# Performance work log

Measured on AMD Instinct MI355X. Metric: run time of the kernel, lower is better.

Reference implementation:

```python
import jax, jax.numpy as jnp
import numpy as np

N_NODES = 20000
N_EDGES = 320000
N_GRAPHS = 512
IN_FEATS = 128
HID = 256
RDKIT_IN = 2048
RDK_H1, RDK_H2 = 1024, 512
COMB_H1, COMB_H2 = 1024, 512
N_TASKS = 1
EPS = 1e-5


def _lin(k, fan_in, fan_out):
    return jax.random.normal(k, (fan_in, fan_out), jnp.float32) / np.float32(np.sqrt(fan_in))


def setup_inputs() -> dict:
    key = jax.random.key(0)
    ks = jax.random.split(key, 24)
    inp = {}
    inp["node_feats"] = jax.random.normal(ks[0], (N_NODES, IN_FEATS), jnp.float32)
    inp["rdkit_feats"] = jax.random.normal(ks[1], (N_GRAPHS, RDKIT_IN), jnp.float32)
    inp["src"] = jax.random.randint(ks[2], (N_EDGES,), 0, N_NODES, dtype=jnp.int32)
    inp["dst"] = jax.random.randint(ks[3], (N_EDGES,), 0, N_NODES, dtype=jnp.int32)
    # sorted graph ids; first N_GRAPHS entries guarantee every graph has >=1 node
    gid = jnp.concatenate([jnp.arange(N_GRAPHS, dtype=jnp.int32),
                           jax.random.randint(ks[4], (N_NODES - N_GRAPHS,), 0, N_GRAPHS, dtype=jnp.int32)])
    inp["node_gid"] = jnp.sort(gid)
    # GCN layer params (GraphConv W,b + residual Linear + BatchNorm gamma/beta)
    dims = [(IN_FEATS, HID), (HID, HID)]
    for i, (fi, fo) in enumerate(dims, start=1):
        inp[f"W{i}"] = _lin(ks[4 + 4 * i], fi, fo)
        inp[f"b{i}"] = jnp.zeros((fo,), jnp.float32)
        inp[f"rW{i}"] = _lin(ks[5 + 4 * i], fi, fo)
        inp[f"rb{i}"] = jnp.zeros((fo,), jnp.float32)
        inp[f"g{i}"] = jnp.ones((fo,), jnp.float32)
        inp[f"be{i}"] = jnp.zeros((fo,), jnp.float32)
    inp["aw_W"] = _lin(ks[16], HID, 1)
    inp["aw_b"] = jnp.zeros((1,), jnp.float32)
    inp["rk_W1"] = _lin(ks[17], RDKIT_IN, RDK_H1)
    inp["rk_b1"] = jnp.zeros((RDK_H1,), jnp.float32)
    inp["rk_W2"] = _lin(ks[18], RDK_H1, RDK_H2)
    inp["rk_b2"] = jnp.zeros((RDK_H2,), jnp.float32)
    comb_in = RDK_H2 + 2 * HID
    inp["c_W1"] = _lin(ks[19], comb_in, COMB_H1)
    inp["c_b1"] = jnp.zeros((COMB_H1,), jnp.float32)
    inp["c_W2"] = _lin(ks[20], COMB_H1, COMB_H2)
    inp["c_b2"] = jnp.zeros((COMB_H2,), jnp.float32)
    inp["c_W3"] = _lin(ks[21], COMB_H2, N_TASKS)
    inp["c_b3"] = jnp.zeros((N_TASKS,), jnp.float32)
    return inp


def _gcn_layer(h, src, dst, W, b, rW, rb, g, be):
    # GraphConv, norm='none': sum incoming messages of (X W), then bias + relu
    m = h @ W                                                    # [N, out]
    agg = jax.ops.segment_sum(m[src], dst, num_segments=h.shape[0])
    new = jax.nn.relu(agg + b)
    # residual Linear with activation (dgllife GCNLayer)
    new = new + jax.nn.relu(h @ rW + rb)
    # BatchNorm1d over nodes (training-mode batch stats; dropout in eval = identity)
    mu = new.mean(axis=0)
    var = new.var(axis=0)
    return g * (new - mu) * jax.lax.rsqrt(var + EPS) + be


def reference(node_feats, rdkit_feats, src, dst, node_gid,
              W1, b1, rW1, rb1, g1, be1,
              W2, b2, rW2, rb2, g2, be2,
              aw_W, aw_b, rk_W1, rk_b1, rk_W2, rk_b2,
              c_W1, c_b1, c_W2, c_b2, c_W3, c_b3):
    h = _gcn_layer(node_feats, src, dst, W1, b1, rW1, rb1, g1, be1)
    h = _gcn_layer(h, src, dst, W2, b2, rW2, rb2, g2, be2)
    # WeightedSumAndMax readout
    w = jax.nn.sigmoid(h @ aw_W + aw_b)                          # [N, 1]
    hg_sum = jax.ops.segment_sum(h * w, node_gid, num_segments=N_GRAPHS)
    hg_max = jax.ops.segment_max(h, node_gid, num_segments=N_GRAPHS)
    graph_feats = jnp.concatenate([hg_sum, hg_max], axis=1)       # [B, 2*HID]
    # RDKit encoder MLP
    r = jax.nn.relu(rdkit_feats @ rk_W1 + rk_b1)
    r = jax.nn.relu(r @ rk_W2 + rk_b2)
    z = jnp.concatenate([graph_feats, r], axis=1)
    z = jax.nn.relu(z @ c_W1 + c_b1)
    z = jax.nn.relu(z @ c_W2 + c_b2)
    return z @ c_W3 + c_b3                                       # [B, n_tasks]
```

## Files before the change

### kernel.cpp

```cpp
#include <hip/hip_runtime.h>
#include <hip/hip_bf16.h>
#include <cstdint>
#include <cstddef>

#define N_NODES 20000
#define N_EDGES 320000
#define N_GRAPHS 512
#define IN_FEATS 128
#define HID 256

typedef __bf16 bhalf;
typedef __bf16 bhalf8 __attribute__((ext_vector_type(8)));
typedef __bf16 bhalf4 __attribute__((ext_vector_type(4)));
typedef __bf16 bhalf2 __attribute__((ext_vector_type(2)));
typedef float f32x4 __attribute__((ext_vector_type(4)));

__device__ __forceinline__ int2 xcd_swz(int bx, int by, int nbx, int nby)
{
    int lid = by * nbx + bx;
    int nwg = nbx * nby;
    int q = nwg >> 3, r = nwg & 7;
    int xcd = lid & 7, loc = lid >> 3;
    int s = (xcd < r ? xcd * (q + 1) : r * (q + 1) + (xcd - r) * q) + loc;
    return make_int2(s % nbx, s / nbx);
}

template<int RELU, int OUTBF16>
__global__ __launch_bounds__(256) void gemm_mfma(const bhalf* __restrict__ A,
                                                 const bhalf* __restrict__ Bt,
                                                 void* __restrict__ Cv,
                                                 const float* __restrict__ bias,
                                                 int M, int K, int ldc)
{
    __shared__ bhalf As[64 * 64];
    __shared__ bhalf Bs[64 * 64];

    const int t = threadIdx.x;
    const int lane = t & 63, wid = t >> 6;
    const int wm0 = (wid >> 1) * 32, wn0 = (wid & 1) * 32;
    int2 bsw = xcd_swz(blockIdx.x, blockIdx.y, gridDim.x, gridDim.y);
    const int m0 = bsw.y * 64, n0 = bsw.x * 64;
    const int S = gridDim.z, kz = blockIdx.z;
    const int Ks = K / S;

    const int srow = t >> 2;
    const int sc0 = (t & 3) << 3;

    f32x4 acc[2][2] = {};
    uint4 ra0, ra1, rb0, rb1;

    const bool mok = (m0 + srow) < M;
    const bhalf* Abase = A + (size_t)(m0 + srow) * K + (size_t)kz * Ks;
    const bhalf* Bbase = Bt + (size_t)(n0 + srow) * K + (size_t)kz * Ks;

    ra0 = mok ? *(const uint4*)(Abase + sc0)      : make_uint4(0u,0u,0u,0u);
    ra1 = mok ? *(const uint4*)(Abase + sc0 + 32) : make_uint4(0u,0u,0u,0u);
    rb0 = *(const uint4*)(Bbase + sc0);
    rb1 = *(const uint4*)(Bbase + sc0 + 32);

    const int swz = (srow & 7) << 3;
    for (int k0 = 0; k0 < Ks; k0 += 64) {
        __syncthreads();
        *(uint4*)&As[srow * 64 + (sc0 ^ swz)]        = ra0;
        *(uint4*)&As[srow * 64 + ((sc0 + 32) ^ swz)] = ra1;
        *(uint4*)&Bs[srow * 64 + (sc0 ^ swz)]        = rb0;
        *(uint4*)&Bs[srow * 64 + ((sc0 + 32) ^ swz)] = rb1;
        __syncthreads();
        if (k0 + 64 < Ks) {
            const bhalf* An = Abase + k0 + 64;
            const bhalf* Bn = Bbase + k0 + 64;
            ra0 = mok ? *(const uint4*)(An + sc0)      : make_uint4(0u,0u,0u,0u);
            ra1 = mok ? *(const uint4*)(An + sc0 + 32) : make_uint4(0u,0u,0u,0u);
            rb0 = *(const uint4*)(Bn + sc0);
            rb1 = *(const uint4*)(Bn + sc0 + 32);
        }
#pragma unroll
        for (int kb = 0; kb < 2; ++kb) {
            const int kc = kb * 32 + (lane >> 4) * 8;
            bhalf8 af[2], bfr[2];
#pragma unroll
            for (int i = 0; i < 2; ++i) {
                int rA = wm0 + i * 16 + (lane & 15);
                af[i] = *(const bhalf8*)&As[rA * 64 + (kc ^ ((rA & 7) << 3))];
                int rB = wn0 + i * 16 + (lane & 15);
                bfr[i] = *(const bhalf8*)&Bs[rB * 64 + (kc ^ ((rB & 7) << 3))];
            }
#pragma unroll
            for (int mi = 0; mi < 2; ++mi)
#pragma unroll
                for (int ni = 0; ni < 2; ++ni)
                    acc[mi][ni] = __builtin_amdgcn_mfma_f32_16x16x32_bf16(
                        af[mi], bfr[ni], acc[mi][ni], 0, 0, 0);
        }
    }

#pragma unroll
    for (int mi = 0; mi < 2; ++mi)
#pragma unroll
        for (int ni = 0; ni < 2; ++ni) {
            int col = n0 + wn0 + ni * 16 + (lane & 15);
            f32x4 v = acc[mi][ni];
            if (S > 1) {
#pragma unroll
                for (int r = 0; r < 4; ++r) {
                    int row = m0 + wm0 + mi * 16 + (lane >> 4) * 4 + r;
                    if (row < M)
                        ((float*)Cv)[((size_t)kz * M + row) * ldc + col] = v[r];
                }
            } else {
                float bb = bias ? bias[col] : 0.f;
#pragma unroll
                for (int r = 0; r < 4; ++r) {
                    int row = m0 + wm0 + mi * 16 + (lane >> 4) * 4 + r;
                    if (row < M) {
                        float x = v[r] + bb;
                        if (RELU) x = fmaxf(x, 0.f);
                        if (OUTBF16) ((bhalf*)Cv)[(size_t)row * ldc + col] = (bhalf)x;
                        else         ((float*)Cv)[(size_t)row * ldc + col] = x;
                    }
                }
            }
        }
}

template<int BN>
__global__ __launch_bounds__(256) void gcn_gemm_fused(const bhalf* __restrict__ Aagg,
                                                      const bhalf* __restrict__ Ax,
                                                      const bhalf* __restrict__ BW,
                                                      const bhalf* __restrict__ BrW,
                                                      const float* __restrict__ b,
                                                      const float* __restrict__ rb,
                                                      bhalf* __restrict__ vout,
                                                      float* __restrict__ stats,
                                                      int M, int K,
                                                      const float* __restrict__ bnstats,
                                                      const float* __restrict__ bng,
                                                      const float* __restrict__ bnbe,
                                                      float inv_n)
{
    __shared__ bhalf As[64 * 64];
    __shared__ bhalf Bs[64 * 64];
    __shared__ float ssum[64], ssq[64];
    __shared__ float bnS[256], bnB[256];

    const int t = threadIdx.x;
    const int lane = t & 63, wid = t >> 6;
    const int wm0 = (wid >> 1) * 32, wn0 = (wid & 1) * 32;
    int2 bsw = xcd_swz(blockIdx.x, blockIdx.y, gridDim.x, gridDim.y);
    const int m0 = bsw.y * 64, n0 = bsw.x * 64;

    const int srow = t >> 2;
    const int sc0 = (t & 3) << 3;
    const int nk = K >> 6;

    if (BN && t < K) {
        float mu = bnstats[t] * inv_n;
        float rs = rsqrtf(bnstats[K + t] * inv_n - mu * mu + 1e-5f);
        float s = bng[t] * rs;
        bnS[t] = s;
        bnB[t] = bnbe[t] - mu * s;
    }

    f32x4 accM[2][2] = {};
    f32x4 accR[2][2] = {};
    uint4 ra0, ra1, rb0, rb1;

    const bool mok = (m0 + srow) < M;
    const bhalf* A0r = Aagg + (size_t)(m0 + srow) * K;
    const bhalf* A1r = Ax + (size_t)(m0 + srow) * K;
    const bhalf* B0r = BW + (size_t)(n0 + srow) * K;
    const bhalf* B1r = BrW + (size_t)(n0 + srow) * K;

    ra0 = mok ? *(const uint4*)(A0r + sc0)      : make_uint4(0u,0u,0u,0u);
    ra1 = mok ? *(const uint4*)(A0r + sc0 + 32) : make_uint4(0u,0u,0u,0u);
    rb0 = *(const uint4*)(B0r + sc0);
    rb1 = *(const uint4*)(B0r + sc0 + 32);

    const int swz = (srow & 7) << 3;
    const int total = 2 * nk;
    if (BN) __syncthreads();
    for (int ii = 0; ii < total; ++ii) {
        __syncthreads();
        if (BN && ii >= nk) {
            int kb0 = ((ii - nk) << 6) + sc0;
            bhalf8 a0 = *(bhalf8*)&ra0, a1 = *(bhalf8*)&ra1;
#pragma unroll
            for (int j = 0; j < 8; ++j) {
                a0[j] = (bhalf)((float)a0[j] * bnS[kb0 + j] + bnB[kb0 + j]);
                a1[j] = (bhalf)((float)a1[j] * bnS[kb0 + 32 + j] + bnB[kb0 + 32 + j]);
            }
            ra0 = *(uint4*)&a0; ra1 = *(uint4*)&a1;
        }
        *(uint4*)&As[srow * 64 + (sc0 ^ swz)]        = ra0;
        *(uint4*)&As[srow * 64 + ((sc0 + 32) ^ swz)] = ra1;
        *(uint4*)&Bs[srow * 64 + (sc0 ^ swz)]        = rb0;
        *(uint4*)&Bs[srow * 64 + ((sc0 + 32) ^ swz)] = rb1;
        __syncthreads();
        int jj = ii + 1;
        if (jj < total) {
            bool seln = jj >= nk;
            int kk = (seln ? jj - nk : jj) << 6;
            const bhalf* Ab = (seln ? A1r : A0r) + kk;
            const bhalf* Bb = (seln ? B1r : B0r) + kk;
            ra0 = mok ? *(const uint4*)(Ab + sc0)      : make_uint4(0u,0u,0u,0u);
            ra1 = mok ? *(const uint4*)(Ab + sc0 + 32) : make_uint4(0u,0u,0u,0u);
            rb0 = *(const uint4*)(Bb + sc0);
            rb1 = *(const uint4*)(Bb + sc0 + 32);
        }
        const bool selc = ii >= nk;
#pragma unroll
        for (int kb = 0; kb < 2; ++kb) {
            const int kc = kb * 32 + (lane >> 4) * 8;
            bhalf8 af[2], bfr[2];
#pragma unroll
            for (int i = 0; i < 2; ++i) {
                int rA = wm0 + i * 16 + (lane & 15);
                af[i] = *(const bhalf8*)&As[rA * 64 + (kc ^ ((rA & 7) << 3))];
                int rB = wn0 + i * 16 + (lane & 15);
                bfr[i] = *(const bhalf8*)&Bs[rB * 64 + (kc ^ ((rB & 7) << 3))];
            }
            if (!selc) {
#pragma unroll
                for (int mi = 0; mi < 2; ++mi)
#pragma unroll
                    for (int ni = 0; ni < 2; ++ni)
                        accM[mi][ni] = __builtin_amdgcn_mfma_f32_16x16x32_bf16(
                            af[mi], bfr[ni], accM[mi][ni], 0, 0, 0);
            } else {
#pragma unroll
                for (int mi = 0; mi < 2; ++mi)
#pragma unroll
                    for (int ni = 0; ni < 2; ++ni)
                        accR[mi][ni] = __builtin_amdgcn_mfma_f32_16x16x32_bf16(
                            af[mi], bfr[ni], accR[mi][ni], 0, 0, 0);
            }
        }
    }

    if (t < 64) { ssum[t] = 0.f; ssq[t] = 0.f; }
    __syncthreads();
    float sloc[2] = {0.f, 0.f}, s2loc[2] = {0.f, 0.f};
#pragma unroll
    for (int ni = 0; ni < 2; ++ni) {
        int cl = wn0 + ni * 16 + (lane & 15);
        int c = n0 + cl;
        float bb = b[c], rbb = rb[c];
#pragma unroll
        for (int mi = 0; mi < 2; ++mi) {
            f32x4 a0v = accM[mi][ni], a1v = accR[mi][ni];
#pragma unroll
            for (int r = 0; r < 4; ++r) {
                int row = m0 + wm0 + mi * 16 + (lane >> 4) * 4 + r;
                if (row < M) {
                    float x = fmaxf(a0v[r] + bb, 0.f) + fmaxf(a1v[r] + rbb, 0.f);
                    vout[(size_t)row * HID + c] = (bhalf)x;
                    sloc[ni] += x;
                    s2loc[ni] += x * x;
                }
            }
        }
        atomicAdd(&ssum[cl], sloc[ni]);
        atomicAdd(&ssq[cl], s2loc[ni]);
    }
    __syncthreads();
    if (t < 64) {
        atomicAdd(&stats[n0 + t], ssum[t]);
        atomicAdd(&stats[HID + n0 + t], ssq[t]);
    }
}

template<int RELU, int OUTBF16>
__global__ __launch_bounds__(256) void splitk_combine(const float* __restrict__ part,
                                                      int S, int M, int N, int ldo,
                                                      const float* __restrict__ bias,
                                                      void* __restrict__ outv)
{
    int i = blockIdx.x * blockDim.x + threadIdx.x;
    int n4 = N >> 2;
    if (i >= M * n4) return;
    int row = i / n4, c4 = (i - row * n4) << 2;
    float4 s = make_float4(0.f, 0.f, 0.f, 0.f);
    for (int z = 0; z < S; ++z) {
        float4 p = *(const float4*)(part + ((size_t)z * M + row) * N + c4);
        s.x += p.x; s.y += p.y; s.z += p.z; s.w += p.w;
    }
    float4 bb = *(const float4*)(bias + c4);
    s.x += bb.x; s.y += bb.y; s.z += bb.z; s.w += bb.w;
    if (RELU) {
        s.x = fmaxf(s.x, 0.f); s.y = fmaxf(s.y, 0.f);
        s.z = fmaxf(s.z, 0.f); s.w = fmaxf(s.w, 0.f);
    }
    if (OUTBF16) {
        bhalf4 o = {(bhalf)s.x, (bhalf)s.y, (bhalf)s.z, (bhalf)s.w};
        *(bhalf4*)((bhalf*)outv + (size_t)row * ldo + c4) = o;
    } else {
        *(float4*)((float*)outv + (size_t)row * ldo + c4) = s;
    }
}

__global__ __launch_bounds__(128) void splitk_combine_dot(const float* __restrict__ part,
                                                          int S, int M, int N,
                                                          const float* __restrict__ bias,
                                                          const float* __restrict__ W3,
                                                          const float* __restrict__ b3,
                                                          float* __restrict__ out)
{
    int row = blockIdx.x, t = threadIdx.x;
    int c4 = t << 2;
    float4 s = make_float4(0.f, 0.f, 0.f, 0.f);
    for (int z = 0; z < S; ++z) {
        float4 p = *(const float4*)(part + ((size_t)z * M + row) * N + c4);
        s.x += p.x; s.y += p.y; s.z += p.z; s.w += p.w;
    }
    float4 bb = *(const float4*)(bias + c4);
    float4 w = *(const float4*)(W3 + c4);
    float d = fmaxf(s.x + bb.x, 0.f) * w.x + fmaxf(s.y + bb.y, 0.f) * w.y
            + fmaxf(s.z + bb.z, 0.f) * w.z + fmaxf(s.w + bb.w, 0.f) * w.w;
#pragma unroll
    for (int off = 32; off > 0; off >>= 1) d += __shfl_xor(d, off);
    __shared__ float ws2[2];
    if ((t & 63) == 0) ws2[t >> 6] = d;
    __syncthreads();
    if (t == 0) out[row] = ws2[0] + ws2[1] + b3[0];
}

struct WEnt { const float* src; bhalf* dst; int K; int N; int tiles_end; };
struct PrepTab {
    WEnt e[8];
    const float* ca; bhalf* coa; int n4a;
    const float* cb; bhalf* cob; int n4b;
    uint4* zbase; int zn;
};

#define WTILES 4288
#define CONVB  3524

__global__ __launch_bounds__(256) void prep_batch(PrepTab tab)
{
    __shared__ float tile[32][33];
    int tb = blockIdx.x;
    int t = threadIdx.x;
    if (tb < WTILES) {
        int idx = 0;
#pragma unroll
        for (int i = 0; i < 8; ++i)
            if (tb >= tab.e[i].tiles_end) idx = i + 1;
        const WEnt& E = tab.e[idx];
        int t0 = idx ? tab.e[idx - 1].tiles_end : 0;
        int lt = tb - t0;
        int tX = E.N >> 5;
        int bx = (lt % tX) << 5;
        int by = (lt / tX) << 5;
        int tx = t & 31, ty = t >> 5;
#pragma unroll
        for (int i = 0; i < 32; i += 8)
            tile[ty + i][tx] = E.src[(size_t)(by + ty + i) * E.N + bx + tx];
        __syncthreads();
#pragma unroll
        for (int i = 0; i < 32; i += 8)
            E.dst[(size_t)(bx + ty + i) * E.K + by + tx] = (bhalf)tile[tx][ty + i];
    } else if (tb < WTILES + CONVB) {
        int i = (tb - WTILES) * 256 + t;
        const float* s; bhalf* d; int j;
        if (i < tab.n4a) { s = tab.ca; d = tab.coa; j = i; }
        else { j = i - tab.n4a; if (j >= tab.n4b) return; s = tab.cb; d = tab.cob; }
        float4 v = ((const float4*)s)[j];
        bhalf4 o = {(bhalf)v.x, (bhalf)v.y, (bhalf)v.z, (bhalf)v.w};
        ((bhalf4*)d)[j] = o;
    } else {
        int j = (tb - WTILES - CONVB) * 256 + t;
        if (j < tab.zn) tab.zbase[j] = make_uint4(0u, 0u, 0u, 0u);
    }
}

__global__ void csr_count(const int* __restrict__ dst, int* __restrict__ counts)
{
    int e = blockIdx.x * blockDim.x + threadIdx.x;
    if (e >= N_EDGES) return;
    atomicAdd(&counts[dst[e]], 1);
}

__global__ __launch_bounds__(256) void csr_scan_a(const int* __restrict__ counts,
                                                  int* __restrict__ bsum)
{
    int i = blockIdx.x * 256 + threadIdx.x;
    int v = (i < N_NODES) ? counts[i] : 0;
#pragma unroll
    for (int off = 32; off > 0; off >>= 1) v += __shfl_down(v, off);
    __shared__ int ws[4];
    if ((threadIdx.x & 63) == 0) ws[threadIdx.x >> 6] = v;
    __syncthreads();
    if (threadIdx.x == 0) bsum[blockIdx.x] = ws[0] + ws[1] + ws[2] + ws[3];
}

__global__ __launch_bounds__(256) void csr_scan_c(const int* __restrict__ counts,
                                                  const int* __restrict__ bsum, int nb,
                                                  int* __restrict__ offsets)
{
    int t = threadIdx.x, b = blockIdx.x;
    int i = b * 256 + t;
    int v = (i < N_NODES) ? counts[i] : 0;
    int x = v;
#pragma unroll
    for (int off = 1; off < 64; off <<= 1) {
        int y = __shfl_up(x, off);
        if ((t & 63) >= off) x += y;
    }
    __shared__ int wsum[4];
    __shared__ int tmp[128];
    __shared__ int addsh;
    if ((t & 63) == 63) wsum[t >> 6] = x;
    if (t < 128) tmp[t] = (t < nb) ? bsum[t] : 0;
    __syncthreads();
    if (t == 0) {
        int a = 0;
        for (int j = 0; j < b; ++j) a += tmp[j];
        addsh = a;
    }
    __syncthreads();
    int add = addsh;
    for (int w = 0; w < (t >> 6); ++w) add += wsum[w];
    int excl = x - v + add;
    if (i < N_NODES) offsets[i] = excl;
    if (i == N_NODES - 1) offsets[N_NODES] = excl + v;
}

__global__ void csr_fill(const int* __restrict__ src, const int* __restrict__ dst,
                         const int* __restrict__ offsets, int* __restrict__ cursor,
                         int* __restrict__ eidx)
{
    int e = blockIdx.x * blockDim.x + threadIdx.x;
    if (e >= N_EDGES) return;
    int d = dst[e];
    int slot = offsets[d] + atomicAdd(&cursor[d], 1);
    eidx[slot] = src[e];
}

__global__ void csr_sort_wave(const int* __restrict__ offsets, int* __restrict__ eidx)
{
    int gidx = blockIdx.x * blockDim.x + threadIdx.x;
    int n = gidx >> 6, lane = gidx & 63;
    if (n >= N_NODES) return;
    int lo = offsets[n], hi = offsets[n + 1];
    int cnt = hi - lo;
    if (cnt <= 1) return;
    if (cnt <= 64) {
        int v = (lane < cnt) ? eidx[lo + lane] : 0x7fffffff;
        int rank = 0;
        for (int j = 0; j < cnt; ++j) {
            int vj = __shfl(v, j);
            if (vj < v || (vj == v && j < lane)) ++rank;
        }
        if (lane < cnt) eidx[lo + rank] = v;
    } else if (lane == 0) {
        for (int i = lo + 1; i < hi; ++i) {
            int v = eidx[i]; int j = i - 1;
            while (j >= lo && eidx[j] > v) { eidx[j + 1] = eidx[j]; --j; }
            eidx[j + 1] = v;
        }
    }
}

__global__ __launch_bounds__(256) void edge_gather1(const bhalf* __restrict__ m,
                                                    const int* __restrict__ offsets,
                                                    const int* __restrict__ eidx,
                                                    bhalf* __restrict__ agg)
{
    int gidx = blockIdx.x * blockDim.x + threadIdx.x;
    int n = gidx >> 6, lane = gidx & 63;
    if (n >= N_NODES) return;
    int lo = offsets[n], hi = offsets[n + 1];
    int sub = lane >> 4;
    int colb = (lane & 15) * 8;
    float acc[8] = {};
    int i = lo;
    for (; i + 8 <= hi; i += 8) {
        bhalf8 v0 = *(const bhalf8*)(m + (size_t)eidx[i + sub] * IN_FEATS + colb);
        bhalf8 v1 = *(const bhalf8*)(m + (size_t)eidx[i + 4 + sub] * IN_FEATS + colb);
#pragma unroll
        for (int j = 0; j < 8; ++j) acc[j] += (float)v0[j] + (float)v1[j];
    }
    if (i + 4 <= hi) {
        bhalf8 v0 = *(const bhalf8*)(m + (size_t)eidx[i + sub] * IN_FEATS + colb);
#pragma unroll
        for (int j = 0; j < 8; ++j) acc[j] += (float)v0[j];
        i += 4;
    }
    if (i < hi && sub < hi - i) {
        bhalf8 v0 = *(const bhalf8*)(m + (size_t)eidx[i + sub] * IN_FEATS + colb);
#pragma unroll
        for (int j = 0; j < 8; ++j) acc[j] += (float)v0[j];
    }
#pragma unroll
    for (int j = 0; j < 8; ++j) {
        acc[j] += __shfl_xor(acc[j], 16);
        acc[j] += __shfl_xor(acc[j], 32);
    }
    if (sub == 0) {
        bhalf8 o;
#pragma unroll
        for (int j = 0; j < 8; ++j) o[j] = (bhalf)acc[j];
        *(bhalf8*)(agg + (size_t)n * IN_FEATS + colb) = o;
    }
}

__global__ __launch_bounds__(256) void edge_gather2_bn(const bhalf* __restrict__ m,
                                                       const int* __restrict__ offsets,
                                                       const int* __restrict__ eidx,
                                                       const float* __restrict__ bnstats,
                                                       const float* __restrict__ bng,
                                                       const float* __restrict__ bnbe,
                                                       float inv_n,
                                                       bhalf* __restrict__ agg)
{
    int gidx = blockIdx.x * blockDim.x + threadIdx.x;
    int n = gidx >> 6, lane = gidx & 63;
    if (n >= N_NODES) return;
    int lo = offsets[n], hi = offsets[n + 1];
    int sub = lane >> 5;
    int colb = (lane & 31) * 8;
    float acc[8] = {};
    int i = lo;
    for (; i + 8 <= hi; i += 8) {
        bhalf8 v0 = *(const bhalf8*)(m + (size_t)eidx[i + sub] * HID + colb);
        bhalf8 v1 = *(const bhalf8*)(m + (size_t)eidx[i + 2 + sub] * HID + colb);
        bhalf8 v2 = *(const bhalf8*)(m + (size_t)eidx[i + 4 + sub] * HID + colb);
        bhalf8 v3 = *(const bhalf8*)(m + (size_t)eidx[i + 6 + sub] * HID + colb);
#pragma unroll
        for (int j = 0; j < 8; ++j)
            acc[j] += ((float)v0[j] + (float)v1[j]) + ((float)v2[j] + (float)v3[j]);
    }
    for (; i + 2 <= hi; i += 2) {
        bhalf8 v0 = *(const bhalf8*)(m + (size_t)eidx[i + sub] * HID + colb);
#pragma unroll
        for (int j = 0; j < 8; ++j) acc[j] += (float)v0[j];
    }
    if (i < hi && sub == 0) {
        bhalf8 v0 = *(const bhalf8*)(m + (size_t)eidx[i] * HID + colb);
#pragma unroll
        for (int j = 0; j < 8; ++j) acc[j] += (float)v0[j];
    }
#pragma unroll
    for (int j = 0; j < 8; ++j)
        acc[j] += __shfl_xor(acc[j], 32);
    if (sub == 0) {
        float d = (float)(hi - lo);
        bhalf8 o;
#pragma unroll
        for (int j = 0; j < 8; ++j) {
            int c = colb + j;
            float mu = bnstats[c] * inv_n;
            float rs = rsqrtf(bnstats[HID + c] * inv_n - mu * mu + 1e-5f);
            float s = bng[c] * rs;
            float tt = bnbe[c] - mu * s;
            o[j] = (bhalf)(acc[j] * s + d * tt);
        }
        *(bhalf8*)(agg + (size_t)n * HID + colb) = o;
    }
}

__global__ __launch_bounds__(256) void bn_row_aw(const bhalf* __restrict__ v,
                                                 const float* __restrict__ stats,
                                                 float inv_n,
                                                 const float* __restrict__ g,
                                                 const float* __restrict__ be,
                                                 bhalf* __restrict__ outb,
                                                 const float* __restrict__ awW,
                                                 const float* __restrict__ awb,
                                                 float* __restrict__ w)
{
    int gidx = blockIdx.x * blockDim.x + threadIdx.x;
    int n = gidx >> 6, lane = gidx & 63;
    if (n >= N_NODES) return;
    int col = lane * 4;
    bhalf4 vv = *(const bhalf4*)(v + (size_t)n * HID + col);
    float4 sm = *(const float4*)(stats + col);
    float4 sq = *(const float4*)(stats + HID + col);
    float4 gg = *(const float4*)(g + col);
    float4 bb = *(const float4*)(be + col);
    float mux = sm.x * inv_n, muy = sm.y * inv_n, muz = sm.z * inv_n, muw = sm.w * inv_n;
    float rsx = rsqrtf(sq.x * inv_n - mux * mux + 1e-5f);
    float rsy = rsqrtf(sq.y * inv_n - muy * muy + 1e-5f);
    float rsz = rsqrtf(sq.z * inv_n - muz * muz + 1e-5f);
    float rsw = rsqrtf(sq.w * inv_n - muw * muw + 1e-5f);
    float4 o;
    o.x = gg.x * ((float)vv.x - mux) * rsx + bb.x;
    o.y = gg.y * ((float)vv.y - muy) * rsy + bb.y;
    o.z = gg.z * ((float)vv.z - muz) * rsz + bb.z;
    o.w = gg.w * ((float)vv.w - muw) * rsw + bb.w;
    bhalf4 ob = {(bhalf)o.x, (bhalf)o.y, (bhalf)o.z, (bhalf)o.w};
    *(bhalf4*)(outb + (size_t)n * HID + col) = ob;
    float4 wv = *(const float4*)(awW + col);
    float d = o.x * wv.x + o.y * wv.y + o.z * wv.z + o.w * wv.w;
#pragma unroll
    for (int off = 32; off > 0; off >>= 1) d += __shfl_xor(d, off);
    if (lane == 0) w[n] = 1.f / (1.f + expf(-(d + awb[0])));
}

__global__ __launch_bounds__(256) void readout(const bhalf* __restrict__ h,
                                               const float* __restrict__ w,
                                               const int* __restrict__ gid,
                                               bhalf* __restrict__ z)
{
    int g = blockIdx.x, col = threadIdx.x;
    int lo = 0, hi = N_NODES;
    while (lo < hi) { int mid = (lo + hi) >> 1; if (gid[mid] < g) lo = mid + 1; else hi = mid; }
    int start = lo;
    hi = N_NODES;
    while (lo < hi) { int mid = (lo + hi) >> 1; if (gid[mid] <= g) lo = mid + 1; else hi = mid; }
    int end = lo;
    float s = 0.f, mx = -INFINITY;
    for (int n = start; n < end; ++n) {
        float v = (float)h[(size_t)n * HID + col];
        s = fmaf(v, w[n], s);
        mx = fmaxf(mx, v);
    }
    z[(size_t)g * 1024 + col] = (bhalf)s;
    z[(size_t)g * 1024 + HID + col] = (bhalf)mx;
}

extern "C" void kernel_launch(void* const* d_in, const int* in_sizes, int n_in,
                              void* d_out, int out_size, void* d_ws, size_t ws_size,
                              hipStream_t stream)
{
    (void)in_sizes; (void)n_in; (void)out_size; (void)ws_size;

    const float* node_feats = (const float*)d_in[0];
    const float* rdkit      = (const float*)d_in[1];
    const int*   src        = (const int*)d_in[2];
    const int*   dst        = (const int*)d_in[3];
    const int*   gid        = (const int*)d_in[4];
    const float* W1  = (const float*)d_in[5];
    const float* b1  = (const float*)d_in[6];
    const float* rW1 = (const float*)d_in[7];
    const float* rb1 = (const float*)d_in[8];
    const float* g1  = (const float*)d_in[9];
    const float* be1 = (const float*)d_in[10];
    const float* W2  = (const float*)d_in[11];
    const float* b2  = (const float*)d_in[12];
    const float* rW2 = (const float*)d_in[13];
    const float* rb2 = (const float*)d_in[14];
    const float* g2  = (const float*)d_in[15];
    const float* be2 = (const float*)d_in[16];
    const float* aw_W  = (const float*)d_in[17];
    const float* aw_b  = (const float*)d_in[18];
    const float* rk_W1 = (const float*)d_in[19];
    const float* rk_b1 = (const float*)d_in[20];
    const float* rk_W2 = (const float*)d_in[21];
    const float* rk_b2 = (const float*)d_in[22];
    const float* c_W1  = (const float*)d_in[23];
    const float* c_b1  = (const float*)d_in[24];
    const float* c_W2  = (const float*)d_in[25];
    const float* c_b2  = (const float*)d_in[26];
    const float* c_W3  = (const float*)d_in[27];
    const float* c_b3  = (const float*)d_in[28];

    float* out = (float*)d_out;

    const size_t NODE = (size_t)N_NODES * HID;
    bhalf* nfb   = (bhalf*)d_ws;
    bhalf* h2b   = nfb + (size_t)N_NODES * IN_FEATS;
    bhalf* aggb  = h2b + NODE;
    bhalf* vb    = aggb + NODE;
    bhalf* vb2   = vb + NODE;
    bhalf* W1cat = vb2 + NODE;
    bhalf* W2cat = W1cat + 512 * 128;
    bhalf* rkW1t = W2cat + 512 * 256;
    bhalf* rkW2t = rkW1t + 2048 * 1024;
    bhalf* cW1t  = rkW2t + 1024 * 512;
    bhalf* cW2t  = cW1t + 1024 * 1024;
    bhalf* rdkb  = cW2t + 1024 * 512;
    float* stats1 = (float*)(rdkb + 512 * 2048);
    float* stats2 = stats1 + 512;
    int*   counts = (int*)(stats2 + 512);
    int*   cursor = counts + N_NODES;
    float* wbuf   = (float*)(cursor + N_NODES);
    int*   offsets = (int*)(wbuf + N_NODES);
    int*   eidx    = offsets + N_NODES + 1;
    int*   bsum    = eidx + N_EDGES;
    bhalf* rkhb  = (bhalf*)(bsum + 128);
    bhalf* zb    = rkhb + 512 * 1024;
    bhalf* ch1b  = zb + 512 * 1024;
    float* spart = (float*)(ch1b + 512 * 1024);

    dim3 blk(256);
    const int EPB = (N_EDGES + 255) / 256;
    const int NPB = (N_NODES + 255) / 256;
    const int NWAVE = (N_NODES * 64) / 256;
    dim3 gfused(HID / 64, (N_NODES + 63) / 64);

    PrepTab tab;
    tab.e[0] = {W1,    W1cat,             128, 256,   32};
    tab.e[1] = {rW1,   W1cat + 256 * 128, 128, 256,   64};
    tab.e[2] = {W2,    W2cat,             256, 256,  128};
    tab.e[3] = {rW2,   W2cat + 256 * 256, 256, 256,  192};
    tab.e[4] = {rk_W1, rkW1t,            2048, 1024, 2240};
    tab.e[5] = {rk_W2, rkW2t,            1024, 512,  2752};
    tab.e[6] = {c_W1,  cW1t,             1024, 1024, 3776};
    tab.e[7] = {c_W2,  cW2t,             1024, 512,  4288};
    tab.ca = node_feats; tab.coa = nfb;  tab.n4a = N_NODES * IN_FEATS / 4;
    tab.cb = rdkit;      tab.cob = rdkb; tab.n4b = 512 * 2048 / 4;
    tab.zbase = (uint4*)stats1;
    tab.zn = (1024 + 2 * N_NODES) / 4;
    const int ZB = (tab.zn + 255) / 256;
    prep_batch<<<WTILES + CONVB + ZB, blk, 0, stream>>>(tab);

    csr_count<<<EPB, blk, 0, stream>>>(dst, counts);
    csr_scan_a<<<NPB, blk, 0, stream>>>(counts, bsum);
    csr_scan_c<<<NPB, blk, 0, stream>>>(counts, bsum, NPB, offsets);
    csr_fill<<<EPB, blk, 0, stream>>>(src, dst, offsets, cursor, eidx);
    csr_sort_wave<<<NWAVE, blk, 0, stream>>>(offsets, eidx);

    edge_gather1<<<NWAVE, blk, 0, stream>>>(nfb, offsets, eidx, aggb);
    gcn_gemm_fused<0><<<gfused, blk, 0, stream>>>(aggb, nfb, W1cat, W1cat + 256 * 128,
                                                  b1, rb1, vb, stats1, N_NODES, IN_FEATS,
                                                  nullptr, nullptr, nullptr, 0.f);

    edge_gather2_bn<<<NWAVE, blk, 0, stream>>>(vb, offsets, eidx,
                                               stats1, g1, be1, 1.0f / N_NODES, aggb);
    gcn_gemm_fused<1><<<gfused, blk, 0, stream>>>(aggb, vb, W2cat, W2cat + 256 * 256,
                                                  b2, rb2, vb2, stats2, N_NODES, HID,
                                                  stats1, g1, be1, 1.0f / N_NODES);
    bn_row_aw<<<NWAVE, blk, 0, stream>>>(vb2, stats2, 1.0f / N_NODES, g2, be2,
                                         h2b, aw_W, aw_b, wbuf);

    readout<<<N_GRAPHS, HID, 0, stream>>>(h2b, wbuf, gid, zb);

    gemm_mfma<0,0><<<dim3(16, 8, 4), blk, 0, stream>>>(rdkb, rkW1t, spart, nullptr,
                                                       512, 2048, 1024);
    splitk_combine<1,1><<<512, blk, 0, stream>>>(spart, 4, 512, 1024, 1024, rk_b1, rkhb);
    gemm_mfma<0,0><<<dim3(8, 8, 8), blk, 0, stream>>>(rkhb, rkW2t, spart, nullptr,
                                                      512, 1024, 512);
    splitk_combine<1,1><<<256, blk, 0, stream>>>(spart, 8, 512, 512, 1024, rk_b2, zb + 512);

    gemm_mfma<0,0><<<dim3(16, 8, 4), blk, 0, stream>>>(zb, cW1t, spart, nullptr,
                                                       512, 1024, 1024);
    splitk_combine<1,1><<<512, blk, 0, stream>>>(spart, 4, 512, 1024, 1024, c_b1, ch1b);
    gemm_mfma<0,0><<<dim3(8, 8, 8), blk, 0, stream>>>(ch1b, cW2t, spart, nullptr,
                                                      512, 1024, 512);
    splitk_combine_dot<<<512, 128, 0, stream>>>(spart, 8, 512, 512, c_b2, c_W3, c_b3, out);
}
```

Baseline: 230.2 us.

## Fuse BN2 and attention weights into readout, fold split-K combine into next GEMM

```diff
diff --git a/kernel.cpp b/kernel.cpp
--- a/kernel.cpp
+++ b/kernel.cpp
@@ -25,11 +25,12 @@
     return make_int2(s % nbx, s / nbx);
 }
 
-template<int RELU, int OUTBF16>
-__global__ __launch_bounds__(256) void gemm_mfma(const bhalf* __restrict__ A,
+template<int RELU, int OUTBF16, int CIN>
+__global__ __launch_bounds__(256) void gemm_mfma(const void* __restrict__ Av,
                                                  const bhalf* __restrict__ Bt,
                                                  void* __restrict__ Cv,
                                                  const float* __restrict__ bias,
+                                                 const float* __restrict__ biasA,
                                                  int M, int K, int ldc)
 {
     __shared__ bhalf As[64 * 64];
@@ -49,28 +50,67 @@
     f32x4 acc[2][2] = {};
     uint4 ra0, ra1, rb0, rb1;
 
-    const bool mok = (m0 + srow) < M;
-    const bhalf* Abase = A + (size_t)(m0 + srow) * K + (size_t)kz * Ks;
+    const int grow = m0 + srow;
+    const bool mok = grow < M;
+    const bhalf* Abase = (const bhalf*)Av + (size_t)grow * K + (size_t)kz * Ks;
+    const float* Afb   = (const float*)Av + (size_t)grow * K + (size_t)kz * Ks;
+    const size_t zstr = (size_t)M * K;
     const bhalf* Bbase = Bt + (size_t)(n0 + srow) * K + (size_t)kz * Ks;
 
-    ra0 = mok ? *(const uint4*)(Abase + sc0)      : make_uint4(0u,0u,0u,0u);
-    ra1 = mok ? *(const uint4*)(Abase + sc0 + 32) : make_uint4(0u,0u,0u,0u);
+    if (CIN == 0) {
+        ra0 = mok ? *(const uint4*)(Abase + sc0)      : make_uint4(0u,0u,0u,0u);
+        ra1 = mok ? *(const uint4*)(Abase + sc0 + 32) : make_uint4(0u,0u,0u,0u);
+    }
     rb0 = *(const uint4*)(Bbase + sc0);
     rb1 = *(const uint4*)(Bbase + sc0 + 32);
 
     const int swz = (srow & 7) << 3;
     for (int k0 = 0; k0 < Ks; k0 += 64) {
         __syncthreads();
-        *(uint4*)&As[srow * 64 + (sc0 ^ swz)]        = ra0;
-        *(uint4*)&As[srow * 64 + ((sc0 + 32) ^ swz)] = ra1;
+        if (CIN == 0) {
+            *(uint4*)&As[srow * 64 + (sc0 ^ swz)]        = ra0;
+            *(uint4*)&As[srow * 64 + ((sc0 + 32) ^ swz)] = ra1;
+        } else {
+            int kg = kz * Ks + k0;
+            float a0[8], a1[8];
+#pragma unroll
+            for (int j = 0; j < 8; ++j) {
+                a0[j] = biasA[kg + sc0 + j];
+                a1[j] = biasA[kg + sc0 + 32 + j];
+            }
+            if (mok) {
+#pragma unroll
+                for (int z = 0; z < CIN; ++z) {
+                    const float* p = Afb + (size_t)z * zstr + k0;
+                    float4 q0 = *(const float4*)(p + sc0);
+                    float4 q1 = *(const float4*)(p + sc0 + 4);
+                    float4 q2 = *(const float4*)(p + sc0 + 32);
+                    float4 q3 = *(const float4*)(p + sc0 + 36);
+                    a0[0] += q0.x; a0[1] += q0.y; a0[2] += q0.z; a0[3] += q0.w;
+                    a0[4] += q1.x; a0[5] += q1.y; a0[6] += q1.z; a0[7] += q1.w;
+                    a1[0] += q2.x; a1[1] += q2.y; a1[2] += q2.z; a1[3] += q2.w;
+                    a1[4] += q3.x; a1[5] += q3.y; a1[6] += q3.z; a1[7] += q3.w;
+                }
+            }
+            bhalf8 o0, o1;
+#pragma unroll
+            for (int j = 0; j < 8; ++j) {
+                o0[j] = (bhalf)(mok ? fmaxf(a0[j], 0.f) : 0.f);
+                o1[j] = (bhalf)(mok ? fmaxf(a1[j], 0.f) : 0.f);
+            }
+            *(bhalf8*)&As[srow * 64 + (sc0 ^ swz)]        = o0;
+            *(bhalf8*)&As[srow * 64 + ((sc0 + 32) ^ swz)] = o1;
+        }
         *(uint4*)&Bs[srow * 64 + (sc0 ^ swz)]        = rb0;
         *(uint4*)&Bs[srow * 64 + ((sc0 + 32) ^ swz)] = rb1;
         __syncthreads();
         if (k0 + 64 < Ks) {
-            const bhalf* An = Abase + k0 + 64;
+            if (CIN == 0) {
+                const bhalf* An = Abase + k0 + 64;
+                ra0 = mok ? *(const uint4*)(An + sc0)      : make_uint4(0u,0u,0u,0u);
+                ra1 = mok ? *(const uint4*)(An + sc0 + 32) : make_uint4(0u,0u,0u,0u);
+            }
             const bhalf* Bn = Bbase + k0 + 64;
-            ra0 = mok ? *(const uint4*)(An + sc0)      : make_uint4(0u,0u,0u,0u);
-            ra1 = mok ? *(const uint4*)(An + sc0 + 32) : make_uint4(0u,0u,0u,0u);
             rb0 = *(const uint4*)(Bn + sc0);
             rb1 = *(const uint4*)(Bn + sc0 + 32);
         }
@@ -559,64 +599,47 @@
     }
 }
 
-__global__ __launch_bounds__(256) void bn_row_aw(const bhalf* __restrict__ v,
-                                                 const float* __restrict__ stats,
-                                                 float inv_n,
-                                                 const float* __restrict__ g,
-                                                 const float* __restrict__ be,
-                                                 bhalf* __restrict__ outb,
-                                                 const float* __restrict__ awW,
-                                                 const float* __restrict__ awb,
-                                                 float* __restrict__ w)
-{
-    int gidx = blockIdx.x * blockDim.x + threadIdx.x;
-    int n = gidx >> 6, lane = gidx & 63;
-    if (n >= N_NODES) return;
-    int col = lane * 4;
-    bhalf4 vv = *(const bhalf4*)(v + (size_t)n * HID + col);
-    float4 sm = *(const float4*)(stats + col);
-    float4 sq = *(const float4*)(stats + HID + col);
-    float4 gg = *(const float4*)(g + col);
-    float4 bb = *(const float4*)(be + col);
-    float mux = sm.x * inv_n, muy = sm.y * inv_n, muz = sm.z * inv_n, muw = sm.w * inv_n;
-    float rsx = rsqrtf(sq.x * inv_n - mux * mux + 1e-5f);
-    float rsy = rsqrtf(sq.y * inv_n - muy * muy + 1e-5f);
-    float rsz = rsqrtf(sq.z * inv_n - muz * muz + 1e-5f);
-    float rsw = rsqrtf(sq.w * inv_n - muw * muw + 1e-5f);
-    float4 o;
-    o.x = gg.x * ((float)vv.x - mux) * rsx + bb.x;
-    o.y = gg.y * ((float)vv.y - muy) * rsy + bb.y;
-    o.z = gg.z * ((float)vv.z - muz) * rsz + bb.z;
-    o.w = gg.w * ((float)vv.w - muw) * rsw + bb.w;
-    bhalf4 ob = {(bhalf)o.x, (bhalf)o.y, (bhalf)o.z, (bhalf)o.w};
-    *(bhalf4*)(outb + (size_t)n * HID + col) = ob;
-    float4 wv = *(const float4*)(awW + col);
-    float d = o.x * wv.x + o.y * wv.y + o.z * wv.z + o.w * wv.w;
-#pragma unroll
-    for (int off = 32; off > 0; off >>= 1) d += __shfl_xor(d, off);
-    if (lane == 0) w[n] = 1.f / (1.f + expf(-(d + awb[0])));
-}
-
-__global__ __launch_bounds__(256) void readout(const bhalf* __restrict__ h,
-                                               const float* __restrict__ w,
-                                               const int* __restrict__ gid,
-                                               bhalf* __restrict__ z)
-{
-    int g = blockIdx.x, col = threadIdx.x;
+__global__ __launch_bounds__(256) void readout_bn(const bhalf* __restrict__ v,
+                                                  const float* __restrict__ stats,
+                                                  float inv_n,
+                                                  const float* __restrict__ g,
+                                                  const float* __restrict__ be,
+                                                  const float* __restrict__ awW,
+                                                  const float* __restrict__ awb,
+                                                  const int* __restrict__ gid,
+                                                  bhalf* __restrict__ z)
+{
+    int gr = blockIdx.x, col = threadIdx.x;
+    int lane = col & 63, wid = col >> 6;
+    float mu = stats[col] * inv_n;
+    float rs = rsqrtf(stats[HID + col] * inv_n - mu * mu + 1e-5f);
+    float s = g[col] * rs;
+    float tt = be[col] - mu * s;
+    float aw = awW[col];
+    float ab = awb[0];
     int lo = 0, hi = N_NODES;
-    while (lo < hi) { int mid = (lo + hi) >> 1; if (gid[mid] < g) lo = mid + 1; else hi = mid; }
+    while (lo < hi) { int mid = (lo + hi) >> 1; if (gid[mid] < gr) lo = mid + 1; else hi = mid; }
     int start = lo;
     hi = N_NODES;
-    while (lo < hi) { int mid = (lo + hi) >> 1; if (gid[mid] <= g) lo = mid + 1; else hi = mid; }
+    while (lo < hi) { int mid = (lo + hi) >> 1; if (gid[mid] <= gr) lo = mid + 1; else hi = mid; }
     int end = lo;
-    float s = 0.f, mx = -INFINITY;
+
+    __shared__ float red[4];
+    float sum = 0.f, mx = -INFINITY;
     for (int n = start; n < end; ++n) {
-        float v = (float)h[(size_t)n * HID + col];
-        s = fmaf(v, w[n], s);
-        mx = fmaxf(mx, v);
-    }
-    z[(size_t)g * 1024 + col] = (bhalf)s;
-    z[(size_t)g * 1024 + HID + col] = (bhalf)mx;
+        float h = (float)v[(size_t)n * HID + col] * s + tt;
+        float d = h * aw;
+#pragma unroll
+        for (int off = 32; off > 0; off >>= 1) d += __shfl_xor(d, off);
+        if (lane == 0) red[wid] = d;
+        __syncthreads();
+        float w = 1.f / (1.f + expf(-(red[0] + red[1] + red[2] + red[3] + ab)));
+        __syncthreads();
+        sum = fmaf(h, w, sum);
+        mx = fmaxf(mx, h);
+    }
+    z[(size_t)gr * 1024 + col] = (bhalf)sum;
+    z[(size_t)gr * 1024 + HID + col] = (bhalf)mx;
 }
 
 extern "C" void kernel_launch(void* const* d_in, const int* in_sizes, int n_in,
@@ -659,8 +682,7 @@
 
     const size_t NODE = (size_t)N_NODES * HID;
     bhalf* nfb   = (bhalf*)d_ws;
-    bhalf* h2b   = nfb + (size_t)N_NODES * IN_FEATS;
-    bhalf* aggb  = h2b + NODE;
+    bhalf* aggb  = nfb + (size_t)N_NODES * IN_FEATS;
     bhalf* vb    = aggb + NODE;
     bhalf* vb2   = vb + NODE;
     bhalf* W1cat = vb2 + NODE;
@@ -674,14 +696,12 @@
     float* stats2 = stats1 + 512;
     int*   counts = (int*)(stats2 + 512);
     int*   cursor = counts + N_NODES;
-    float* wbuf   = (float*)(cursor + N_NODES);
-    int*   offsets = (int*)(wbuf + N_NODES);
+    int*   offsets = cursor + N_NODES;
     int*   eidx    = offsets + N_NODES + 1;
     int*   bsum    = eidx + N_EDGES;
-    bhalf* rkhb  = (bhalf*)(bsum + 128);
-    bhalf* zb    = rkhb + 512 * 1024;
-    bhalf* ch1b  = zb + 512 * 1024;
-    float* spart = (float*)(ch1b + 512 * 1024);
+    bhalf* zb    = (bhalf*)(bsum + 128);
+    float* spart = (float*)(zb + 512 * 1024);
+    float* spart2 = spart + 4 * 512 * 1024;
 
     dim3 blk(256);
     const int EPB = (N_EDGES + 255) / 256;
@@ -721,22 +741,19 @@
     gcn_gemm_fused<1><<<gfused, blk, 0, stream>>>(aggb, vb, W2cat, W2cat + 256 * 256,
                                                   b2, rb2, vb2, stats2, N_NODES, HID,
                                                   stats1, g1, be1, 1.0f / N_NODES);
-    bn_row_aw<<<NWAVE, blk, 0, stream>>>(vb2, stats2, 1.0f / N_NODES, g2, be2,
-                                         h2b, aw_W, aw_b, wbuf);
-
-    readout<<<N_GRAPHS, HID, 0, stream>>>(h2b, wbuf, gid, zb);
-
-    gemm_mfma<0,0><<<dim3(16, 8, 4), blk, 0, stream>>>(rdkb, rkW1t, spart, nullptr,
-                                                       512, 2048, 1024);
-    splitk_combine<1,1><<<512, blk, 0, stream>>>(spart, 4, 512, 1024, 1024, rk_b1, rkhb);
-    gemm_mfma<0,0><<<dim3(8, 8, 8), blk, 0, stream>>>(rkhb, rkW2t, spart, nullptr,
-                                                      512, 1024, 512);
-    splitk_combine<1,1><<<256, blk, 0, stream>>>(spart, 8, 512, 512, 1024, rk_b2, zb + 512);
-
-    gemm_mfma<0,0><<<dim3(16, 8, 4), blk, 0, stream>>>(zb, cW1t, spart, nullptr,
-                                                       512, 1024, 1024);
-    splitk_combine<1,1><<<512, blk, 0, stream>>>(spart, 4, 512, 1024, 1024, c_b1, ch1b);
-    gemm_mfma<0,0><<<dim3(8, 8, 8), blk, 0, stream>>>(ch1b, cW2t, spart, nullptr,
-                                                      512, 1024, 512);
-    splitk_combine_dot<<<512, 128, 0, stream>>>(spart, 8, 512, 512, c_b2, c_W3, c_b3, out);
-}
+
+    readout_bn<<<N_GRAPHS, HID, 0, stream>>>(vb2, stats2, 1.0f / N_NODES, g2, be2,
+                                             aw_W, aw_b, gid, zb);
+
+    gemm_mfma<0,0,0><<<dim3(16, 8, 4), blk, 0, stream>>>(rdkb, rkW1t, spart, nullptr,
+                                                         nullptr, 512, 2048, 1024);
+    gemm_mfma<0,0,4><<<dim3(8, 8, 8), blk, 0, stream>>>(spart, rkW2t, spart2, nullptr,
+                                                        rk_b1, 512, 1024, 512);
+    splitk_combine<1,1><<<256, blk, 0, stream>>>(spart2, 8, 512, 512, 1024, rk_b2, zb + 512);
+
+    gemm_mfma<0,0,0><<<dim3(16, 8, 4), blk, 0, stream>>>(zb, cW1t, spart, nullptr,
+                                                         nullptr, 512, 1024, 1024);
+    gemm_mfma<0,0,4><<<dim3(8, 8, 8), blk, 0, stream>>>(spart, cW2t, spart2, nullptr,
+                                                        c_b1, 512, 1024, 512);
+    splitk_combine_dot<<<512, 128, 0, stream>>>(spart2, 8, 512, 512, c_b2, c_W3, c_b3, out);
+}
```

Result: slower. 238.6 us (+3.6%).
